# Performance work log

Measured on AMD Instinct MI355X. Metric: run time of the kernel, lower is better.

The kernel has to match this reference:

```python
import jax, jax.numpy as jnp
import numpy as np
from jax import lax

SAMPLE_RATE = 44100.0

def _shelf_coeffs(gain_db, fc, q, sr, high):
    # RBJ cookbook shelf biquad; high=True -> high_shelf, else low_shelf
    A = 10.0 ** (gain_db / 40.0)
    w0 = 2.0 * jnp.pi * (fc / sr)
    alpha = jnp.sin(w0) / (2.0 * q)
    c = jnp.cos(w0)
    sA = jnp.sqrt(A)
    sgn = 1.0 if high else -1.0
    b0 = A * (A + 1 + sgn * (A - 1) * c + 2 * sA * alpha)
    b1 = -2.0 * sgn * A * (A - 1 + sgn * (A + 1) * c)
    b2 = A * (A + 1 + sgn * (A - 1) * c - 2 * sA * alpha)
    a0 = A + 1 - sgn * (A - 1) * c + 2 * sA * alpha
    a1 = 2.0 * sgn * (A - 1 - sgn * (A + 1) * c)
    a2 = A + 1 - sgn * (A - 1) * c - 2 * sA * alpha
    b = jnp.stack([b0, b1, b2]) / a0
    a = jnp.stack([a0, a1, a2]) / a0
    return b, a

def _peaking_coeffs(gain_db, fc, q, sr):
    A = 10.0 ** (gain_db / 40.0)
    w0 = 2.0 * jnp.pi * (fc / sr)
    alpha = jnp.sin(w0) / (2.0 * q)
    c = jnp.cos(w0)
    b0 = 1 + alpha * A
    b1 = -2.0 * c
    b2 = 1 - alpha * A
    a0 = 1 + alpha / A
    a1 = -2.0 * c
    a2 = 1 - alpha / A
    b = jnp.stack([b0, b1, b2]) / a0
    a = jnp.stack([a0, a1, a2]) / a0
    return b, a

def _biquad_lfilter(b, a, x):
    # scipy.signal.lfilter with zero initial conditions, transposed DF-II.
    # x: (chs, T); state s: (chs, 2)
    b0, b1, b2 = b[0], b[1], b[2]
    a1, a2 = a[1], a[2]
    def step(s, xn):  # xn: (chs,)
        s1, s2 = s[:, 0], s[:, 1]
        yn = b0 * xn + s1
        s1n = b1 * xn - a1 * yn + s2
        s2n = b2 * xn - a2 * yn
        return jnp.stack([s1n, s2n], axis=1), yn
    s0 = jnp.zeros((x.shape[0], 2), x.dtype)
    _, y = lax.scan(step, s0, x.T)  # y: (T, chs)
    return y.T

def setup_inputs() -> dict:
    key = jax.random.key(0)
    x = jax.random.normal(key, (8, 2097152), dtype=jnp.float32)
    # rows: [low_shelf, band1, band2, band3, high_shelf]; cols: [gain_db, cutoff_hz, Q]
    eq_params = jnp.array([
        [3.0, 100.0, 0.9],
        [-2.5, 400.0, 1.2],
        [4.0, 1000.0, 2.0],
        [-5.0, 4000.0, 0.7],
        [2.5, 12000.0, 0.707],
    ], dtype=jnp.float32)
    return {"x": x, "eq_params": eq_params}

def reference(x, eq_params):
    sr = SAMPLE_RATE
    # low shelf
    b, a = _shelf_coeffs(eq_params[0, 0], eq_params[0, 1], eq_params[0, 2], sr, high=False)
    y = _biquad_lfilter(b, a, x)
    # 3 peaking bands
    for i in range(1, 4):
        b, a = _peaking_coeffs(eq_params[i, 0], eq_params[i, 1], eq_params[i, 2], sr)
        y = _biquad_lfilter(b, a, y)
    # high shelf
    b, a = _shelf_coeffs(eq_params[4, 0], eq_params[4, 1], eq_params[4, 2], sr, high=True)
    y = _biquad_lfilter(b, a, y)
    return y.astype(jnp.float32)
```

## Files before the change

### kernel.cpp

```cpp
#include <hip/hip_runtime.h>

#define SRATE 44100.0
#define L_CHUNK 256
#define SAMPLES_PER_CH 2097152
#define CHUNKS_PER_CH 8192
#define NCH 8
#define TOTAL_CHUNKS 65536
#define NBLK 256
#define BLK_PER_CH 32
#define NWIN 16
#define WIN 16
#define STRIDE 17

#ifndef M_PI
#define M_PI 3.14159265358979323846
#endif

struct CoefD { double b0, b1, b2, a1, a2; };

__device__ void cascade_step_d(const CoefD* cf, double* s, double x) {
    double u = x;
    #pragma unroll
    for (int i = 0; i < 5; i++) {
        double y   = cf[i].b0 * u + s[2*i];
        double s1n = cf[i].b1 * u - cf[i].a1 * y + s[2*i+1];
        double s2n = cf[i].b2 * u - cf[i].a2 * y;
        s[2*i]   = s1n;
        s[2*i+1] = s2n;
        u = y;
    }
}

__global__ __launch_bounds__(128) void k0_setup(const float* __restrict__ eqp,
                                                float* __restrict__ coef_f,
                                                float* __restrict__ mats_f) {
    __shared__ CoefD cf[5];
    __shared__ double M[100];
    int t = threadIdx.x;

    if (t == 0) {
        for (int i = 0; i < 5; i++) {
            double g  = (double)eqp[i*3 + 0];
            double fc = (double)eqp[i*3 + 1];
            double q  = (double)eqp[i*3 + 2];
            double A  = pow(10.0, g / 40.0);
            double w0 = 2.0 * M_PI * (fc / SRATE);
            double al = sin(w0) / (2.0 * q);
            double c  = cos(w0);
            double b0, b1, b2, a0, a1, a2;
            if (i == 0 || i == 4) {
                double sgn = (i == 4) ? 1.0 : -1.0;
                double sA = sqrt(A);
                b0 = A * ((A + 1.0) + sgn * (A - 1.0) * c + 2.0 * sA * al);
                b1 = -2.0 * sgn * A * ((A - 1.0) + sgn * (A + 1.0) * c);
                b2 = A * ((A + 1.0) + sgn * (A - 1.0) * c - 2.0 * sA * al);
                a0 = (A + 1.0) - sgn * (A - 1.0) * c + 2.0 * sA * al;
                a1 = 2.0 * sgn * ((A - 1.0) - sgn * (A + 1.0) * c);
                a2 = (A + 1.0) - sgn * (A - 1.0) * c - 2.0 * sA * al;
            } else {
                b0 = 1.0 + al * A; b1 = -2.0 * c; b2 = 1.0 - al * A;
                a0 = 1.0 + al / A; a1 = -2.0 * c; a2 = 1.0 - al / A;
            }
            cf[i].b0 = b0 / a0; cf[i].b1 = b1 / a0; cf[i].b2 = b2 / a0;
            cf[i].a1 = a1 / a0; cf[i].a2 = a2 / a0;
            coef_f[i*5 + 0] = (float)(b0 / a0);
            coef_f[i*5 + 1] = (float)(b1 / a0);
            coef_f[i*5 + 2] = (float)(b2 / a0);
            coef_f[i*5 + 3] = (float)(a1 / a0);
            coef_f[i*5 + 4] = (float)(a2 / a0);
        }
    }
    __syncthreads();

    if (t < 10) {
        double s[10];
        for (int k = 0; k < 10; k++) s[k] = (k == t) ? 1.0 : 0.0;
        cascade_step_d(cf, s, 0.0);
        for (int r = 0; r < 10; r++) M[r*10 + t] = s[r];
    }
    __syncthreads();

    for (int k = 1; k <= 20; k++) {
        double val = 0.0;
        if (t < 100) {
            int r = t / 10, c = t % 10;
            for (int j = 0; j < 10; j++) val += M[r*10 + j] * M[j*10 + c];
        }
        __syncthreads();
        if (t < 100) {
            M[t] = val;
            if (k >= 8 && k <= 15)  mats_f[(k-8)*100 + t]        = (float)val;
            if (k >= 16)            mats_f[800 + (k-16)*100 + t] = (float)val;
        }
        __syncthreads();
    }
}

__global__ __launch_bounds__(256) void k1_partial(const float* __restrict__ x,
                                                  const float* __restrict__ coef,
                                                  float* __restrict__ cbuf) {
    __shared__ float inb[2][256 * STRIDE];
    int t = threadIdx.x, b = blockIdx.x;

    float cb0[5], cb1[5], cb2[5], ca1[5], ca2[5];
    #pragma unroll
    for (int i = 0; i < 5; i++) {
        cb0[i] = coef[i*5+0]; cb1[i] = coef[i*5+1]; cb2[i] = coef[i*5+2];
        ca1[i] = coef[i*5+3]; ca2[i] = coef[i*5+4];
    }
    const float4* x4 = (const float4*)x;
    const size_t base4 = (size_t)b * 16384;
    const int cb = t >> 2, q = t & 3;

    float4 rr[4];
    #pragma unroll
    for (int k = 0; k < 4; k++)
        rr[k] = x4[base4 + (size_t)(cb + 64*k) * 64 + q];
    #pragma unroll
    for (int k = 0; k < 4; k++) {
        int o = (cb + 64*k) * STRIDE + q*4;
        inb[0][o+0] = rr[k].x; inb[0][o+1] = rr[k].y;
        inb[0][o+2] = rr[k].z; inb[0][o+3] = rr[k].w;
    }
    __syncthreads();

    float s[10];
    #pragma unroll
    for (int k = 0; k < 10; k++) s[k] = 0.0f;

    for (int w = 0; w < NWIN; w++) {
        if (w + 1 < NWIN) {
            #pragma unroll
            for (int k = 0; k < 4; k++)
                rr[k] = x4[base4 + (size_t)(cb + 64*k) * 64 + (w+1)*4 + q];
        }
        const float* cur = inb[w & 1] + t * STRIDE;
        #pragma unroll
        for (int i = 0; i < WIN; i++) {
            float u = cur[i];
            #pragma unroll
            for (int st = 0; st < 5; st++) {
                float y  = fmaf(cb0[st], u, s[2*st]);
                float t1 = fmaf(cb1[st], u, s[2*st+1]);
                s[2*st+1] = fmaf(-ca2[st], y, cb2[st] * u);
                s[2*st]   = fmaf(-ca1[st], y, t1);
                u = y;
            }
        }
        __syncthreads();
        if (w + 1 < NWIN) {
            float* nb = inb[(w+1) & 1];
            #pragma unroll
            for (int k = 0; k < 4; k++) {
                int o = (cb + 64*k) * STRIDE + q*4;
                nb[o+0] = rr[k].x; nb[o+1] = rr[k].y;
                nb[o+2] = rr[k].z; nb[o+3] = rr[k].w;
            }
        }
        __syncthreads();
    }
    #pragma unroll
    for (int r = 0; r < 10; r++)
        cbuf[(size_t)b * 2560 + r * 256 + t] = s[r];
}

__global__ __launch_bounds__(256) void k2a_scan(const float* __restrict__ mats_f,
                                                const float* __restrict__ cbuf,
                                                float* __restrict__ ibuf,
                                                float* __restrict__ abuf) {
    __shared__ float Mds[800];
    __shared__ float buf[256][11];
    int t = threadIdx.x, b = blockIdx.x;

    for (int i = t; i < 800; i += 256) Mds[i] = mats_f[i];

    float v[10];
    #pragma unroll
    for (int r = 0; r < 10; r++) {
        v[r] = cbuf[(size_t)b * 2560 + r * 256 + t];
        buf[t][r] = v[r];
    }
    __syncthreads();

    for (int d = 0; d < 8; d++) {
        float nv[10];
        bool act = (t >= (1 << d));
        if (act) {
            int src = t - (1 << d);
            #pragma unroll
            for (int r = 0; r < 10; r++) {
                float acc = v[r];
                #pragma unroll
                for (int k = 0; k < 10; k++)
                    acc = fmaf(Mds[d*100 + r*10 + k], buf[src][k], acc);
                nv[r] = acc;
            }
        }
        __syncthreads();
        if (act) {
            #pragma unroll
            for (int r = 0; r < 10; r++) { v[r] = nv[r]; buf[t][r] = nv[r]; }
        }
        __syncthreads();
    }

    #pragma unroll
    for (int r = 0; r < 10; r++)
        ibuf[(size_t)b * 2560 + r * 256 + t] = (t > 0) ? buf[t-1][r] : 0.0f;
    if (t == 255) {
        #pragma unroll
        for (int r = 0; r < 10; r++) abuf[b * 10 + r] = v[r];
    }
}

__global__ __launch_bounds__(256) void k2b_scan(const float* __restrict__ mats_f,
                                                const float* __restrict__ abuf,
                                                float* __restrict__ bbuf) {
    __shared__ float Qds[500];
    __shared__ float buf[256][11];
    int t = threadIdx.x;
    int i = t & 31;

    for (int k = t; k < 500; k += 256) Qds[k] = mats_f[800 + k];

    float v[10];
    #pragma unroll
    for (int r = 0; r < 10; r++) { v[r] = abuf[t * 10 + r]; buf[t][r] = v[r]; }
    __syncthreads();

    for (int e = 0; e < 5; e++) {
        float nv[10];
        bool act = (i >= (1 << e));
        if (act) {
            int src = t - (1 << e);
            #pragma unroll
            for (int r = 0; r < 10; r++) {
                float acc = v[r];
                #pragma unroll
                for (int k = 0; k < 10; k++)
                    acc = fmaf(Qds[e*100 + r*10 + k], buf[src][k], acc);
                nv[r] = acc;
            }
        }
        __syncthreads();
        if (act) {
            #pragma unroll
            for (int r = 0; r < 10; r++) { v[r] = nv[r]; buf[t][r] = nv[r]; }
        }
        __syncthreads();
    }
    #pragma unroll
    for (int r = 0; r < 10; r++)
        bbuf[t * 10 + r] = (i > 0) ? buf[t-1][r] : 0.0f;
}

__global__ __launch_bounds__(256) void k3_final(const float* __restrict__ x,
                                                const float* __restrict__ coef,
                                                const float* __restrict__ mats_f,
                                                const float* __restrict__ ibuf,
                                                const float* __restrict__ bbuf,
                                                float* __restrict__ out) {
    __shared__ float inb[2][256 * STRIDE];
    __shared__ float outb[256 * STRIDE];
    __shared__ float Mds[800];
    int t = threadIdx.x, b = blockIdx.x;

    const float4* x4 = (const float4*)x;
    float4* o4 = (float4*)out;
    const size_t base4 = (size_t)b * 16384;
    const int cb = t >> 2, q = t & 3;

    float4 rr[4];
    #pragma unroll
    for (int k = 0; k < 4; k++)
        rr[k] = x4[base4 + (size_t)(cb + 64*k) * 64 + q];

    for (int i = t; i < 800; i += 256) Mds[i] = mats_f[i];

    float cb0[5], cb1[5], cb2[5], ca1[5], ca2[5];
    #pragma unroll
    for (int i = 0; i < 5; i++) {
        cb0[i] = coef[i*5+0]; cb1[i] = coef[i*5+1]; cb2[i] = coef[i*5+2];
        ca1[i] = coef[i*5+3]; ca2[i] = coef[i*5+4];
    }

    float s[10];
    #pragma unroll
    for (int r = 0; r < 10; r++)
        s[r] = ibuf[(size_t)b * 2560 + r * 256 + t];

    float v[10];
    #pragma unroll
    for (int r = 0; r < 10; r++) v[r] = bbuf[b * 10 + r];

    #pragma unroll
    for (int k = 0; k < 4; k++) {
        int o = (cb + 64*k) * STRIDE + q*4;
        inb[0][o+0] = rr[k].x; inb[0][o+1] = rr[k].y;
        inb[0][o+2] = rr[k].z; inb[0][o+3] = rr[k].w;
    }
    __syncthreads();

    for (int d = 0; d < 8; d++) {
        float wv[10];
        #pragma unroll
        for (int r = 0; r < 10; r++) {
            float acc = 0.0f;
            #pragma unroll
            for (int k = 0; k < 10; k++)
                acc = fmaf(Mds[d*100 + r*10 + k], v[k], acc);
            wv[r] = acc;
        }
        bool bit = (t >> d) & 1;
        #pragma unroll
        for (int r = 0; r < 10; r++) v[r] = bit ? wv[r] : v[r];
    }
    #pragma unroll
    for (int r = 0; r < 10; r++) s[r] += v[r];

    for (int w = 0; w < NWIN; w++) {
        if (w + 1 < NWIN) {
            #pragma unroll
            for (int k = 0; k < 4; k++)
                rr[k] = x4[base4 + (size_t)(cb + 64*k) * 64 + (w+1)*4 + q];
        }
        const float* cur = inb[w & 1] + t * STRIDE;
        float* orow = outb + t * STRIDE;
        #pragma unroll
        for (int i = 0; i < WIN; i++) {
            float u = cur[i];
            #pragma unroll
            for (int st = 0; st < 5; st++) {
                float y  = fmaf(cb0[st], u, s[2*st]);
                float t1 = fmaf(cb1[st], u, s[2*st+1]);
                s[2*st+1] = fmaf(-ca2[st], y, cb2[st] * u);
                s[2*st]   = fmaf(-ca1[st], y, t1);
                u = y;
            }
            orow[i] = u;
        }
        __syncthreads();

        #pragma unroll
        for (int k = 0; k < 4; k++) {
            int o = (cb + 64*k) * STRIDE + q*4;
            float4 ov = make_float4(outb[o+0], outb[o+1], outb[o+2], outb[o+3]);
            o4[base4 + (size_t)(cb + 64*k) * 64 + (size_t)w*4 + q] = ov;
        }
        if (w + 1 < NWIN) {
            float* nb = inb[(w+1) & 1];
            #pragma unroll
            for (int k = 0; k < 4; k++) {
                int o = (cb + 64*k) * STRIDE + q*4;
                nb[o+0] = rr[k].x; nb[o+1] = rr[k].y;
                nb[o+2] = rr[k].z; nb[o+3] = rr[k].w;
            }
        }
        __syncthreads();
    }
}

extern "C" void kernel_launch(void* const* d_in, const int* in_sizes, int n_in,
                              void* d_out, int out_size, void* d_ws, size_t ws_size,
                              hipStream_t stream) {
    const float* x   = (const float*)d_in[0];
    const float* eqp = (const float*)d_in[1];
    float* out = (float*)d_out;
    char* ws = (char*)d_ws;

    float* coef_f = (float*)ws;
    float* mats_f = (float*)(ws + 256);
    float* cbuf   = (float*)(ws + 8192);
    float* ibuf   = (float*)(ws + 8192 + 2621440);
    float* abuf   = (float*)(ws + 8192 + 2*2621440);
    float* bbuf   = (float*)(ws + 8192 + 2*2621440 + 16384);

    hipLaunchKernelGGL(k0_setup, dim3(1), dim3(128), 0, stream, eqp, coef_f, mats_f);
    hipLaunchKernelGGL(k1_partial, dim3(NBLK), dim3(256), 0, stream, x, coef_f, cbuf);
    hipLaunchKernelGGL(k2a_scan, dim3(NBLK), dim3(256), 0, stream, mats_f, cbuf, ibuf, abuf);
    hipLaunchKernelGGL(k2b_scan, dim3(1), dim3(256), 0, stream, mats_f, abuf, bbuf);
    hipLaunchKernelGGL(k3_final, dim3(NBLK), dim3(256), 0, stream,
                       x, coef_f, mats_f, ibuf, bbuf, out);
}
```

Baseline: 170.1 us.

## Fuse partial-state and block-scan kernels, shrink chunks to 64 samples, quadruple block count

Merges the chunk-state pass and the intra-block scan into one kernel that reuses shared memory through a union, removing the cbuf round trip and one launch. Chunk length drops from 256 to 64 samples, so there are 1024 blocks instead of 256, the matrix powers shift accordingly, and the cross-block scan grows to 7 levels over 128 blocks per channel. The final kernel writes outputs in place in the input staging buffer, dropping the separate output buffer, and occupancy hints are added. The trade-off is more chunk-boundary state (the ibuf scratch grows fourfold) and more scan work, in exchange for better GPU fill and fewer serial samples per thread.

Result: slower. 174.3 us (+2.4%).

```diff
diff --git a/kernel.cpp b/kernel.cpp
--- a/kernel.cpp
+++ b/kernel.cpp
@@ -1,16 +1,11 @@
 #include <hip/hip_runtime.h>
 
 #define SRATE 44100.0
-#define L_CHUNK 256
-#define SAMPLES_PER_CH 2097152
-#define CHUNKS_PER_CH 8192
-#define NCH 8
-#define TOTAL_CHUNKS 65536
-#define NBLK 256
-#define BLK_PER_CH 32
-#define NWIN 16
 #define WIN 16
+#define NWIN 4
 #define STRIDE 17
+#define NBLK 1024
+#define BLK_PER_CH 128
 
 #ifndef M_PI
 #define M_PI 3.14159265358979323846
@@ -89,17 +84,22 @@
         __syncthreads();
         if (t < 100) {
             M[t] = val;
-            if (k >= 8 && k <= 15)  mats_f[(k-8)*100 + t]        = (float)val;
-            if (k >= 16)            mats_f[800 + (k-16)*100 + t] = (float)val;
-        }
-        __syncthreads();
-    }
-}
-
-__global__ __launch_bounds__(256) void k1_partial(const float* __restrict__ x,
-                                                  const float* __restrict__ coef,
-                                                  float* __restrict__ cbuf) {
-    __shared__ float inb[2][256 * STRIDE];
+            if (k >= 6 && k <= 13) mats_f[(k-6)*100 + t]         = (float)val;
+            if (k >= 14)           mats_f[800 + (k-14)*100 + t]  = (float)val;
+        }
+        __syncthreads();
+    }
+}
+
+__global__ __launch_bounds__(256, 4) void k1_fused(const float* __restrict__ x,
+                                                   const float* __restrict__ coef,
+                                                   const float* __restrict__ mats_f,
+                                                   float* __restrict__ ibuf,
+                                                   float* __restrict__ abuf) {
+    __shared__ union SmemU {
+        float stage[2][256 * STRIDE];
+        struct { float M[800]; float buf[256][11]; } scan;
+    } sm;
     int t = threadIdx.x, b = blockIdx.x;
 
     float cb0[5], cb1[5], cb2[5], ca1[5], ca2[5];
@@ -109,18 +109,18 @@
         ca1[i] = coef[i*5+3]; ca2[i] = coef[i*5+4];
     }
     const float4* x4 = (const float4*)x;
-    const size_t base4 = (size_t)b * 16384;
+    const size_t base4 = (size_t)b * 4096;
     const int cb = t >> 2, q = t & 3;
 
     float4 rr[4];
     #pragma unroll
     for (int k = 0; k < 4; k++)
-        rr[k] = x4[base4 + (size_t)(cb + 64*k) * 64 + q];
+        rr[k] = x4[base4 + (size_t)(cb + 64*k) * 16 + q];
     #pragma unroll
     for (int k = 0; k < 4; k++) {
         int o = (cb + 64*k) * STRIDE + q*4;
-        inb[0][o+0] = rr[k].x; inb[0][o+1] = rr[k].y;
-        inb[0][o+2] = rr[k].z; inb[0][o+3] = rr[k].w;
+        sm.stage[0][o+0] = rr[k].x; sm.stage[0][o+1] = rr[k].y;
+        sm.stage[0][o+2] = rr[k].z; sm.stage[0][o+3] = rr[k].w;
     }
     __syncthreads();
 
@@ -132,9 +132,9 @@
         if (w + 1 < NWIN) {
             #pragma unroll
             for (int k = 0; k < 4; k++)
-                rr[k] = x4[base4 + (size_t)(cb + 64*k) * 64 + (w+1)*4 + q];
-        }
-        const float* cur = inb[w & 1] + t * STRIDE;
+                rr[k] = x4[base4 + (size_t)(cb + 64*k) * 16 + (w+1)*4 + q];
+        }
+        const float* cur = sm.stage[w & 1] + t * STRIDE;
         #pragma unroll
         for (int i = 0; i < WIN; i++) {
             float u = cur[i];
@@ -147,9 +147,8 @@
                 u = y;
             }
         }
-        __syncthreads();
         if (w + 1 < NWIN) {
-            float* nb = inb[(w+1) & 1];
+            float* nb = sm.stage[(w+1) & 1];
             #pragma unroll
             for (int k = 0; k < 4; k++) {
                 int o = (cb + 64*k) * STRIDE + q*4;
@@ -159,27 +158,10 @@
         }
         __syncthreads();
     }
-    #pragma unroll
-    for (int r = 0; r < 10; r++)
-        cbuf[(size_t)b * 2560 + r * 256 + t] = s[r];
-}
-
-__global__ __launch_bounds__(256) void k2a_scan(const float* __restrict__ mats_f,
-                                                const float* __restrict__ cbuf,
-                                                float* __restrict__ ibuf,
-                                                float* __restrict__ abuf) {
-    __shared__ float Mds[800];
-    __shared__ float buf[256][11];
-    int t = threadIdx.x, b = blockIdx.x;
-
-    for (int i = t; i < 800; i += 256) Mds[i] = mats_f[i];
-
-    float v[10];
-    #pragma unroll
-    for (int r = 0; r < 10; r++) {
-        v[r] = cbuf[(size_t)b * 2560 + r * 256 + t];
-        buf[t][r] = v[r];
-    }
+
+    for (int i = t; i < 800; i += 256) sm.scan.M[i] = mats_f[i];
+    #pragma unroll
+    for (int r = 0; r < 10; r++) sm.scan.buf[t][r] = s[r];
     __syncthreads();
 
     for (int d = 0; d < 8; d++) {
@@ -189,48 +171,48 @@
             int src = t - (1 << d);
             #pragma unroll
             for (int r = 0; r < 10; r++) {
-                float acc = v[r];
+                float acc = s[r];
                 #pragma unroll
                 for (int k = 0; k < 10; k++)
-                    acc = fmaf(Mds[d*100 + r*10 + k], buf[src][k], acc);
+                    acc = fmaf(sm.scan.M[d*100 + r*10 + k], sm.scan.buf[src][k], acc);
                 nv[r] = acc;
             }
         }
         __syncthreads();
         if (act) {
             #pragma unroll
-            for (int r = 0; r < 10; r++) { v[r] = nv[r]; buf[t][r] = nv[r]; }
+            for (int r = 0; r < 10; r++) { s[r] = nv[r]; sm.scan.buf[t][r] = nv[r]; }
         }
         __syncthreads();
     }
 
     #pragma unroll
     for (int r = 0; r < 10; r++)
-        ibuf[(size_t)b * 2560 + r * 256 + t] = (t > 0) ? buf[t-1][r] : 0.0f;
+        ibuf[(size_t)b * 2560 + r * 256 + t] = (t > 0) ? sm.scan.buf[t-1][r] : 0.0f;
     if (t == 255) {
         #pragma unroll
-        for (int r = 0; r < 10; r++) abuf[b * 10 + r] = v[r];
-    }
-}
-
-__global__ __launch_bounds__(256) void k2b_scan(const float* __restrict__ mats_f,
+        for (int r = 0; r < 10; r++) abuf[b * 10 + r] = s[r];
+    }
+}
+
+__global__ __launch_bounds__(128) void k2b_scan(const float* __restrict__ mats_f,
                                                 const float* __restrict__ abuf,
                                                 float* __restrict__ bbuf) {
-    __shared__ float Qds[500];
-    __shared__ float buf[256][11];
-    int t = threadIdx.x;
-    int i = t & 31;
-
-    for (int k = t; k < 500; k += 256) Qds[k] = mats_f[800 + k];
+    __shared__ float Qds[700];
+    __shared__ float buf[128][11];
+    int t = threadIdx.x, ch = blockIdx.x;
+    int g = ch * 128 + t;
+
+    for (int k = t; k < 700; k += 128) Qds[k] = mats_f[800 + k];
 
     float v[10];
     #pragma unroll
-    for (int r = 0; r < 10; r++) { v[r] = abuf[t * 10 + r]; buf[t][r] = v[r]; }
-    __syncthreads();
-
-    for (int e = 0; e < 5; e++) {
+    for (int r = 0; r < 10; r++) { v[r] = abuf[g * 10 + r]; buf[t][r] = v[r]; }
+    __syncthreads();
+
+    for (int e = 0; e < 7; e++) {
         float nv[10];
-        bool act = (i >= (1 << e));
+        bool act = (t >= (1 << e));
         if (act) {
             int src = t - (1 << e);
             #pragma unroll
@@ -251,29 +233,28 @@
     }
     #pragma unroll
     for (int r = 0; r < 10; r++)
-        bbuf[t * 10 + r] = (i > 0) ? buf[t-1][r] : 0.0f;
-}
-
-__global__ __launch_bounds__(256) void k3_final(const float* __restrict__ x,
-                                                const float* __restrict__ coef,
-                                                const float* __restrict__ mats_f,
-                                                const float* __restrict__ ibuf,
-                                                const float* __restrict__ bbuf,
-                                                float* __restrict__ out) {
+        bbuf[g * 10 + r] = (t > 0) ? buf[t-1][r] : 0.0f;
+}
+
+__global__ __launch_bounds__(256, 4) void k3_final(const float* __restrict__ x,
+                                                   const float* __restrict__ coef,
+                                                   const float* __restrict__ mats_f,
+                                                   const float* __restrict__ ibuf,
+                                                   const float* __restrict__ bbuf,
+                                                   float* __restrict__ out) {
     __shared__ float inb[2][256 * STRIDE];
-    __shared__ float outb[256 * STRIDE];
     __shared__ float Mds[800];
     int t = threadIdx.x, b = blockIdx.x;
 
     const float4* x4 = (const float4*)x;
     float4* o4 = (float4*)out;
-    const size_t base4 = (size_t)b * 16384;
+    const size_t base4 = (size_t)b * 4096;
     const int cb = t >> 2, q = t & 3;
 
     float4 rr[4];
     #pragma unroll
     for (int k = 0; k < 4; k++)
-        rr[k] = x4[base4 + (size_t)(cb + 64*k) * 64 + q];
+        rr[k] = x4[base4 + (size_t)(cb + 64*k) * 16 + q];
 
     for (int i = t; i < 800; i += 256) Mds[i] = mats_f[i];
 
@@ -288,7 +269,6 @@
     #pragma unroll
     for (int r = 0; r < 10; r++)
         s[r] = ibuf[(size_t)b * 2560 + r * 256 + t];
-
     float v[10];
     #pragma unroll
     for (int r = 0; r < 10; r++) v[r] = bbuf[b * 10 + r];
@@ -322,10 +302,9 @@
         if (w + 1 < NWIN) {
             #pragma unroll
             for (int k = 0; k < 4; k++)
-                rr[k] = x4[base4 + (size_t)(cb + 64*k) * 64 + (w+1)*4 + q];
-        }
-        const float* cur = inb[w & 1] + t * STRIDE;
-        float* orow = outb + t * STRIDE;
+                rr[k] = x4[base4 + (size_t)(cb + 64*k) * 16 + (w+1)*4 + q];
+        }
+        float* cur = inb[w & 1] + t * STRIDE;
         #pragma unroll
         for (int i = 0; i < WIN; i++) {
             float u = cur[i];
@@ -337,15 +316,7 @@
                 s[2*st]   = fmaf(-ca1[st], y, t1);
                 u = y;
             }
-            orow[i] = u;
-        }
-        __syncthreads();
-
-        #pragma unroll
-        for (int k = 0; k < 4; k++) {
-            int o = (cb + 64*k) * STRIDE + q*4;
-            float4 ov = make_float4(outb[o+0], outb[o+1], outb[o+2], outb[o+3]);
-            o4[base4 + (size_t)(cb + 64*k) * 64 + (size_t)w*4 + q] = ov;
+            cur[i] = u;
         }
         if (w + 1 < NWIN) {
             float* nb = inb[(w+1) & 1];
@@ -357,6 +328,14 @@
             }
         }
         __syncthreads();
+
+        const float* sb = inb[w & 1];
+        #pragma unroll
+        for (int k = 0; k < 4; k++) {
+            int o = (cb + 64*k) * STRIDE + q*4;
+            float4 ov = make_float4(sb[o+0], sb[o+1], sb[o+2], sb[o+3]);
+            o4[base4 + (size_t)(cb + 64*k) * 16 + (size_t)w*4 + q] = ov;
+        }
     }
 }
 
@@ -370,15 +349,13 @@
 
     float* coef_f = (float*)ws;
     float* mats_f = (float*)(ws + 256);
-    float* cbuf   = (float*)(ws + 8192);
-    float* ibuf   = (float*)(ws + 8192 + 2621440);
-    float* abuf   = (float*)(ws + 8192 + 2*2621440);
-    float* bbuf   = (float*)(ws + 8192 + 2*2621440 + 16384);
+    float* ibuf   = (float*)(ws + 8192);
+    float* abuf   = (float*)(ws + 8192 + 10485760);
+    float* bbuf   = (float*)(ws + 8192 + 10485760 + 40960);
 
     hipLaunchKernelGGL(k0_setup, dim3(1), dim3(128), 0, stream, eqp, coef_f, mats_f);
-    hipLaunchKernelGGL(k1_partial, dim3(NBLK), dim3(256), 0, stream, x, coef_f, cbuf);
-    hipLaunchKernelGGL(k2a_scan, dim3(NBLK), dim3(256), 0, stream, mats_f, cbuf, ibuf, abuf);
-    hipLaunchKernelGGL(k2b_scan, dim3(1), dim3(256), 0, stream, mats_f, abuf, bbuf);
+    hipLaunchKernelGGL(k1_fused, dim3(NBLK), dim3(256), 0, stream, x, coef_f, mats_f, ibuf, abuf);
+    hipLaunchKernelGGL(k2b_scan, dim3(8), dim3(128), 0, stream, mats_f, abuf, bbuf);
     hipLaunchKernelGGL(k3_final, dim3(NBLK), dim3(256), 0, stream,
                        x, coef_f, mats_f, ibuf, bbuf, out);
 }
```
